# Kernel tuning notes

Measured on AMD Instinct MI355X. Metric: run time of the kernel, lower is better.

## Reference

```python
import jax, jax.numpy as jnp
import numpy as np

EPSILON = 0.01  # mesh.epsilon: boundary band of the unit square


def setup_inputs() -> dict:
    key = jax.random.key(0)
    k1, k2, k3 = jax.random.split(key, 3)
    V, E, F = 50000, 150000, 128
    image = jax.random.normal(k1, (V, F), dtype=jnp.float32)
    vs = jax.random.uniform(k2, (V, 2), dtype=jnp.float32)
    edges = jax.random.randint(k3, (2, E), 0, V, dtype=jnp.int32)
    return {"image": image, "vs": vs, "edges": edges, "out_target": 25000}


def _edge_priority(image, edges):
    # features = cat(image[e0], image[e1], dim=1) -> [E, 2F]; priority = ||f||^2 per edge
    f0 = image[edges[0]]  # [E, F]
    f1 = image[edges[1]]  # [E, F]
    return jnp.sum(f0 * f0, axis=1) + jnp.sum(f1 * f1, axis=1)  # [E]


def _boundary_mask(vs, edges):
    v0 = vs[edges[0]]  # [E, 2]
    v1 = vs[edges[1]]  # [E, 2]
    def near_border(v):
        return (v[:, 0] < EPSILON) | (v[:, 0] > 1 - EPSILON) | (v[:, 1] < EPSILON) | (v[:, 1] > 1 - EPSILON)
    return near_border(v0) | near_border(v1)  # [E] bool


def reference(image, vs, edges, out_target):
    V = image.shape[0]
    sq = _edge_priority(image, edges)            # [E] float32 (heap keys)
    is_boundary = _boundary_mask(vs, edges)      # [E] bool

    # heappop order == ascending priority (ties broken by edge id, matching heapify on [value, id])
    order = jnp.argsort(sq)
    e0 = edges[0][order]
    e1 = edges[1][order]
    bnd = is_boundary[order]

    # Sequential greedy edge collapse: pop min edge; if both endpoints alive and
    # not a boundary edge, merge (kill edges[1] vertex) until vertex_count hits target.
    def step(carry, x):
        mask, count = carry
        v0, v1, b = x
        alive = mask[v0] & mask[v1]
        do = (count > out_target) & alive & (~b)
        mask = mask.at[v1].set(jnp.where(do, False, mask[v1]))
        count = count - do.astype(jnp.int32)
        return (mask, count), None

    init = (jnp.ones((V,), dtype=bool), jnp.int32(V))
    (vertex_mask, vertex_count), _ = jax.lax.scan(step, init, (e0, e1, bnd))
    return sq, vertex_mask, vertex_count
```

## Files before the change

kernel.cpp:

```cpp
#include <hip/hip_runtime.h>
#include <hip/hip_bf16.h>
#include <stdint.h>

typedef unsigned int u32;
typedef unsigned long long u64;
typedef unsigned char u8;
typedef unsigned short u16;


__global__ __launch_bounds__(256) void vnorm_kernel(const float* __restrict__ image,
                                                    float* __restrict__ nrm, int V) {
#pragma clang fp contract(off)
  int t = blockIdx.x * 256 + threadIdx.x;
  int v = t >> 1, h = t & 1;
  if (v >= V) return;
  const float4* r4 = (const float4*)(image + (size_t)v * 128) + h;
  float4 a, x;
  x = r4[0];
  a.x = x.x * x.x; a.y = x.y * x.y; a.z = x.z * x.z; a.w = x.w * x.w;
#pragma unroll
  for (int i = 1; i < 16; ++i) {
    x = r4[i * 2];
    a.x = a.x + x.x * x.x; a.y = a.y + x.y * x.y;
    a.z = a.z + x.z * x.z; a.w = a.w + x.w * x.w;
  }
  float bx = __shfl_xor(a.x, 1), by = __shfl_xor(a.y, 1);
  float bz = __shfl_xor(a.z, 1), bw = __shfl_xor(a.w, 1);
  a.x = a.x + bx; a.y = a.y + by; a.z = a.z + bz; a.w = a.w + bw;
  float r0 = a.x + a.z;
  float r1 = a.y + a.w;
  float s = r0 + r1;
  if (h == 0) nrm[v] = s;
}

__global__ __launch_bounds__(256) void edge_kernel(const float* __restrict__ nrm,
                                                   const float* __restrict__ vs,
                                                   const int* __restrict__ edges,
                                                   u64* __restrict__ keysA,
                                                   u8* __restrict__ bnd,
                                                   float* __restrict__ out_sq,
                                                   u32* __restrict__ gmm, int E) {
#pragma clang fp contract(off)
  __shared__ u32 smn[4], smx[4];
  int tid = threadIdx.x;
  int e = blockIdx.x * 256 + tid;
  u32 mn = 0xFFFFFFFFu, mx = 0u;
  if (e < E) {
    int v0 = edges[e], v1 = edges[E + e];
    float sq = nrm[v0] + nrm[v1];
    out_sq[e] = sq;
    u32 sb = __float_as_uint(sq);
    keysA[e] = ((u64)sb << 32) | (u32)e;
    float ax = vs[2 * v0], ay = vs[2 * v0 + 1];
    float bx = vs[2 * v1], by = vs[2 * v1 + 1];
    const float lo = 0.01f, hi = 0.99f;
    bool b = (ax < lo) | (ax > hi) | (ay < lo) | (ay > hi)
           | (bx < lo) | (bx > hi) | (by < lo) | (by > hi);
    bnd[e] = b ? 1 : 0;
    mn = sb; mx = sb;
  }
  int lane = tid & 63, wv = tid >> 6;
#pragma unroll
  for (int d = 32; d >= 1; d >>= 1) {
    u32 a = __shfl_xor(mn, d); mn = (a < mn) ? a : mn;
    u32 b2 = __shfl_xor(mx, d); mx = (b2 > mx) ? b2 : mx;
  }
  if (lane == 0) { smn[wv] = mn; smx[wv] = mx; }
  __syncthreads();
  if (tid == 0) {
    u32 m = smn[0], M = smx[0];
#pragma unroll
    for (int w = 1; w < 4; ++w) {
      if (smn[w] < m) m = smn[w];
      if (smx[w] > M) M = smx[w];
    }
    atomicMin(&gmm[0], m);
    atomicMax(&gmm[1], M);
  }
}

__device__ inline u32 bucket_of(u32 sb, u32 minv, u32 range) {
  return (u32)(((u64)(sb - minv) << 14) / ((u64)range + 1ull));
}

__global__ __launch_bounds__(256) void hist_kernel(const u64* __restrict__ keysA,
                                                   const u32* __restrict__ gmm,
                                                   u32* __restrict__ ghist, int E) {
  int e = blockIdx.x * 256 + threadIdx.x;
  if (e >= E) return;
  u32 minv = gmm[0], range = gmm[1] - minv;
  u32 b = bucket_of((u32)(keysA[e] >> 32), minv, range);
  atomicAdd(&ghist[b], 1u);
}

__global__ __launch_bounds__(1024) void scan16k_kernel(const u32* __restrict__ ghist,
                                                       u32* __restrict__ starts,
                                                       u32* __restrict__ cursor, int E) {
  __shared__ u32 wsum[16];
  int tid = threadIdx.x;
  int lane = tid & 63, wv = tid >> 6;
  u32 loc[16];
  u32 s = 0;
#pragma unroll
  for (int i = 0; i < 16; ++i) { loc[i] = ghist[tid * 16 + i]; s += loc[i]; }
  u32 inc = s;
#pragma unroll
  for (int d = 1; d < 64; d <<= 1) {
    u32 t = __shfl_up(inc, d);
    if (lane >= d) inc += t;
  }
  if (lane == 63) wsum[wv] = inc;
  __syncthreads();
  if (tid == 0) {
    u32 r = 0;
#pragma unroll
    for (int w = 0; w < 16; ++w) { u32 t = wsum[w]; wsum[w] = r; r += t; }
  }
  __syncthreads();
  u32 run = wsum[wv] + (inc - s);
#pragma unroll
  for (int i = 0; i < 16; ++i) {
    starts[tid * 16 + i] = run;
    cursor[tid * 16 + i] = run;
    run += loc[i];
  }
  if (tid == 0) starts[16384] = (u32)E;
}

__global__ __launch_bounds__(256) void scatter_kernel(const u64* __restrict__ keysA,
                                                      const u32* __restrict__ gmm,
                                                      u32* __restrict__ cursor,
                                                      u64* __restrict__ keysB, int E) {
  int e = blockIdx.x * 256 + threadIdx.x;
  if (e >= E) return;
  u64 key = keysA[e];
  u32 minv = gmm[0], range = gmm[1] - minv;
  u32 b = bucket_of((u32)(key >> 32), minv, range);
  u32 pos = atomicAdd(&cursor[b], 1u);
  keysB[pos] = key;
}

__global__ __launch_bounds__(256) void bucketsort_kernel(const u64* __restrict__ keysB,
                                                         const u32* __restrict__ starts,
                                                         const int* __restrict__ edges,
                                                         const u8* __restrict__ bnd,
                                                         u64* __restrict__ pack,
                                                         int E, int V, int Npad) {
  int tid = threadIdx.x;
  int lane = tid & 63;
  int w = blockIdx.x * 4 + (tid >> 6);
  u32 start = starts[w];
  int cnt = (int)(starts[w + 1] - start);
  if (cnt > 128) cnt = 128;
  u64 k0 = (lane < cnt) ? keysB[start + lane] : ~0ull;
  u64 k1 = (64 + lane < cnt) ? keysB[start + 64 + lane] : ~0ull;
  int idx0 = lane * 2, idx1 = lane * 2 + 1;
#pragma unroll
  for (int k = 2; k <= 128; k <<= 1) {
#pragma unroll
    for (int j = 64; j >= 1; j >>= 1) {
      if (j > k / 2) continue;
      if (j >= 2) {
        int lj = j >> 1;
        u64 p0 = __shfl_xor(k0, lj);
        u64 p1 = __shfl_xor(k1, lj);
        bool keepMin0 = (((idx0 & j) == 0) == ((idx0 & k) == 0));
        k0 = keepMin0 ? (k0 < p0 ? k0 : p0) : (k0 > p0 ? k0 : p0);
        k1 = keepMin0 ? (k1 < p1 ? k1 : p1) : (k1 > p1 ? k1 : p1);
      } else {
        bool up = ((idx0 & k) == 0);
        u64 mn = (k0 < k1) ? k0 : k1;
        u64 mx = (k0 < k1) ? k1 : k0;
        k0 = up ? mn : mx;
        k1 = up ? mx : mn;
      }
    }
  }
  if (idx0 < cnt) {
    u32 id = (u32)k0;
    int vv0 = edges[id], vv1 = edges[E + id];
    pack[start + idx0] = (u64)(u32)(vv0 | (vv1 << 16)) | ((u64)bnd[id] << 32);
  }
  if (idx1 < cnt) {
    u32 id = (u32)k1;
    int vv0 = edges[id], vv1 = edges[E + id];
    pack[start + idx1] = (u64)(u32)(vv0 | (vv1 << 16)) | ((u64)bnd[id] << 32);
  }
  int g = blockIdx.x * 256 + tid;
  int i = E + g;
  if (i < Npad) {
    u32 sv0 = (u32)V + (((u32)i & 255u) << 1);
    pack[i] = (u64)(sv0 | ((sv0 + 1) << 16)) | (1ull << 32);
  }
}

__device__ inline void lds_min_u16(u16* tarr, int idx, u16 val) {
  u32* w = (u32*)(tarr + (idx & ~1));
  int sh = (idx & 1) * 16;
  u32 old = *w;
  while (true) {
    u32 cur = (old >> sh) & 0xffffu;
    if ((u32)val >= cur) break;
    u32 nv = (old & ~(0xffffu << sh)) | ((u32)val << sh);
    u32 prev = atomicCAS(w, old, nv);
    if (prev == old) break;
    old = prev;
  }
}

__global__ __launch_bounds__(1024) void batch_kernel(const u64* __restrict__ pack,
                                                     const int* __restrict__ tgt,
                                                     float* __restrict__ out,
                                                     u32* __restrict__ gbits,
                                                     int V, int E, int Npad) {
  __shared__ u16 tUK[50560];
  __shared__ u32 alive[1600];
  __shared__ u32 wred[17];
  __shared__ u32 misc[4];
  int tid = threadIdx.x;
  int lane = tid & 63, wv = tid >> 6;
  for (int i = tid; i < 1600; i += 1024) alive[i] = 0xFFFFFFFFu;
  for (int i = tid; i < 25280; i += 1024) ((u32*)tUK)[i] = 0xFFFFFFFFu;
  if (tid < 4) misc[tid] = 0u;
  int target = tgt[0];
  int needed = V - target; if (needed < 0) needed = 0;
  int remaining = needed;
  __syncthreads();
  int nbatch = Npad / 1024;
  u64 pk = pack[tid];
  for (int b = 0; b < nbatch; ++b) {
    if (remaining <= 0) break;
    u64 pkn = (b + 1 < nbatch) ? pack[(b + 1) * 1024 + tid] : pk;
    int v0 = (int)(pk & 0xffff), v1 = (int)((pk >> 16) & 0xffff);
    int nb = (int)((pk >> 32) & 1);
    int a0 = (int)((alive[v0 >> 5] >> (v0 & 31)) & 1);
    int a1 = (int)((alive[v1 >> 5] >> (v1 & 31)) & 1);
    int und = a0 & a1 & (nb ^ 1);
    int kill = 0;
    u32 myval = ((u32)tid << 1) | 1u;
    for (int r = 0; r < 1100; ++r) {
      if (und | kill) lds_min_u16(tUK, v1, (u16)(((u32)tid << 1) | (u32)und));
      __syncthreads();
      int newk = 0, newnk = 0;
      if (und) {
        u32 b0v = (v0 == v1) ? 0xFFFFu : (u32)tUK[v0];
        u32 b1v = (u32)tUK[v1];
        int ek = (int)(((b0v < myval) & ((b0v & 1u) ^ 1u)) |
                       ((b1v < myval) & ((b1v & 1u) ^ 1u)));
        int c0 = (int)(b0v > myval);
        int c1 = (int)(b1v == myval);
        newk = c0 & c1 & (ek ^ 1);
        newnk = ek;
      }
      kill |= newk;
      und &= (newk | newnk) ^ 1;
      u64 au = __ballot(und);
      if (lane == 0 && au) atomicOr(&misc[r & 3], 1u);
      if (tid == 0) misc[(r + 2) & 3] = 0u;
      __syncthreads();
      tUK[v1] = 0xFFFF;
      u32 anyu = misc[r & 3];
      __syncthreads();
      if (anyu == 0u) break;
    }
    u64 km = __ballot(kill);
    if (lane == 0) wred[wv] = (u32)__popcll(km);
    __syncthreads();
    if (tid == 0) {
      u32 run = 0;
      for (int w = 0; w < 16; ++w) { u32 t2 = wred[w]; wred[w] = run; run += t2; }
      wred[16] = run;
    }
    __syncthreads();
    u32 K = wred[16];
    if (kill) {
      u32 rank = wred[wv] + (u32)__popcll(km & ((1ull << lane) - 1ull));
      if (rank < (u32)remaining)
        atomicAnd(&alive[v1 >> 5], ~(1u << (v1 & 31)));
    }
    remaining -= (int)((K < (u32)remaining) ? K : (u32)remaining);
    if (tid < 4) misc[tid] = 0u;
    __syncthreads();
    pk = pkn;
  }
  for (int i = tid; i < 1600; i += 1024) gbits[i] = alive[i];
  if (tid == 0) out[E + V] = (float)(V - (needed - remaining));
}

__global__ __launch_bounds__(256) void expand_kernel(const u32* __restrict__ gbits,
                                                     float* __restrict__ out,
                                                     int V, int E) {
  int i = blockIdx.x * 256 + threadIdx.x;
  if (i < V) out[E + i] = ((gbits[i >> 5] >> (i & 31)) & 1) ? 1.0f : 0.0f;
}

extern "C" void kernel_launch(void* const* d_in, const int* in_sizes, int n_in,
                              void* d_out, int out_size, void* d_ws, size_t ws_size,
                              hipStream_t stream) {
  const float* image = (const float*)d_in[0];
  const float* vs    = (const float*)d_in[1];
  const int*   edges = (const int*)d_in[2];
  const int*   tgt   = (const int*)d_in[3];
  int V = in_sizes[1] / 2;
  int E = in_sizes[2] / 2;
  int Npad = ((E + 1023) / 1024) * 1024;

  char* ws = (char*)d_ws;
  size_t o = 0;
  u64* keysA  = (u64*)(ws + o); o += (size_t)E * 8;
  u64* keysB  = (u64*)(ws + o); o += (size_t)E * 8;
  u64* pack   = (u64*)(ws + o); o += (size_t)Npad * 8;
  float* nrm  = (float*)(ws + o); o += (size_t)V * 4;
  u8*  bnd    = (u8*)(ws + o);  o += (size_t)E;
  o = (o + 255) & ~(size_t)255;
  u32* ghist  = (u32*)(ws + o); o += 16384 * 4;
  u32* starts = (u32*)(ws + o); o += 16385 * 4;
  u32* cursor = (u32*)(ws + o); o += 16384 * 4;
  u32* gbits  = (u32*)(ws + o); o += 6400;
  u32* gmm    = (u32*)(ws + o); o += 256;
  float* out = (float*)d_out;

  (void)hipMemsetAsync(ghist, 0, 16384 * 4, stream);
  (void)hipMemsetAsync(&gmm[0], 0xFF, 4, stream);
  (void)hipMemsetAsync(&gmm[1], 0x00, 4, stream);

  int eb = (E + 255) / 256;
  vnorm_kernel<<<dim3((2 * V + 255) / 256), dim3(256), 0, stream>>>(image, nrm, V);
  edge_kernel<<<dim3(eb), dim3(256), 0, stream>>>(nrm, vs, edges, keysA, bnd, out, gmm, E);
  hist_kernel<<<dim3(eb), dim3(256), 0, stream>>>(keysA, gmm, ghist, E);
  scan16k_kernel<<<dim3(1), dim3(1024), 0, stream>>>(ghist, starts, cursor, E);
  scatter_kernel<<<dim3(eb), dim3(256), 0, stream>>>(keysA, gmm, cursor, keysB, E);
  bucketsort_kernel<<<dim3(4096), dim3(256), 0, stream>>>(keysB, starts, edges, bnd,
                                                          pack, E, V, Npad);
  batch_kernel<<<dim3(1), dim3(1024), 0, stream>>>(pack, tgt, out, gbits, V, E, Npad);
  expand_kernel<<<dim3((V + 255) / 256), dim3(256), 0, stream>>>(gbits, out, V, E);
}
```

Before: 261.0 us.

## Process 4096 edges per greedy batch and fold expand into batch kernel

The single-block greedy collapse now resolves 4096 sorted edges per batch instead of 1024. Each thread owns four edges, using macro-unrolled post/decide/rank/apply phases and a 64-entry warp-prefix array. This cuts the number of sequential batches and their barrier-heavy setup, but each batch may need more conflict-resolution rounds, and every round does four times the LDS work per thread. The separate expand kernel and its gbits buffer are removed, and the alive bitmask is written straight to the output from shared memory.

```diff
diff --git a/kernel.cpp b/kernel.cpp
--- a/kernel.cpp
+++ b/kernel.cpp
@@ -145,7 +145,7 @@
                                                          const int* __restrict__ edges,
                                                          const u8* __restrict__ bnd,
                                                          u64* __restrict__ pack,
-                                                         int E, int V, int Npad) {
+                                                         int E, int V, int NpadB) {
   int tid = threadIdx.x;
   int lane = tid & 63;
   int w = blockIdx.x * 4 + (tid >> 6);
@@ -188,7 +188,7 @@
   }
   int g = blockIdx.x * 256 + tid;
   int i = E + g;
-  if (i < Npad) {
+  if (i < NpadB) {
     u32 sv0 = (u32)V + (((u32)i & 255u) << 1);
     pack[i] = (u64)(sv0 | ((sv0 + 1) << 16)) | (1ull << 32);
   }
@@ -208,14 +208,15 @@
   }
 }
 
+#define NBAT 4096
+
 __global__ __launch_bounds__(1024) void batch_kernel(const u64* __restrict__ pack,
                                                      const int* __restrict__ tgt,
                                                      float* __restrict__ out,
-                                                     u32* __restrict__ gbits,
-                                                     int V, int E, int Npad) {
+                                                     int V, int E, int NpadB) {
   __shared__ u16 tUK[50560];
   __shared__ u32 alive[1600];
-  __shared__ u32 wred[17];
+  __shared__ u32 wred[65];
   __shared__ u32 misc[4];
   int tid = threadIdx.x;
   int lane = tid & 63, wv = tid >> 6;
@@ -226,72 +227,74 @@
   int needed = V - target; if (needed < 0) needed = 0;
   int remaining = needed;
   __syncthreads();
-  int nbatch = Npad / 1024;
-  u64 pk = pack[tid];
+  int nbatch = NpadB / NBAT;
+  u64 pk0 = pack[tid],        pk1 = pack[1024 + tid];
+  u64 pk2 = pack[2048 + tid], pk3 = pack[3072 + tid];
   for (int b = 0; b < nbatch; ++b) {
     if (remaining <= 0) break;
-    u64 pkn = (b + 1 < nbatch) ? pack[(b + 1) * 1024 + tid] : pk;
-    int v0 = (int)(pk & 0xffff), v1 = (int)((pk >> 16) & 0xffff);
-    int nb = (int)((pk >> 32) & 1);
-    int a0 = (int)((alive[v0 >> 5] >> (v0 & 31)) & 1);
-    int a1 = (int)((alive[v1 >> 5] >> (v1 & 31)) & 1);
-    int und = a0 & a1 & (nb ^ 1);
-    int kill = 0;
-    u32 myval = ((u32)tid << 1) | 1u;
-    for (int r = 0; r < 1100; ++r) {
-      if (und | kill) lds_min_u16(tUK, v1, (u16)(((u32)tid << 1) | (u32)und));
+    const u64* np = pack + (size_t)((b + 1 < nbatch) ? (b + 1) : b) * NBAT;
+    u64 pn0 = np[tid],        pn1 = np[1024 + tid];
+    u64 pn2 = np[2048 + tid], pn3 = np[3072 + tid];
+#define BDEC(S) \
+    int v0##S = (int)(pk##S & 0xffff), w1##S = (int)((pk##S >> 16) & 0xffff); \
+    int und##S, kill##S = 0; \
+    { int nb_ = (int)((pk##S >> 32) & 1); \
+      int a0 = (int)((alive[v0##S >> 5] >> (v0##S & 31)) & 1); \
+      int a1 = (int)((alive[w1##S >> 5] >> (w1##S & 31)) & 1); \
+      und##S = a0 & a1 & (nb_ ^ 1); } \
+    u32 my##S = ((u32)(S * 1024 + tid) << 1) | 1u;
+    BDEC(0) BDEC(1) BDEC(2) BDEC(3)
+    for (int r = 0; r < 4200; ++r) {
+#define BPOST(S) if (und##S | kill##S) \
+      lds_min_u16(tUK, w1##S, (u16)((((u32)(S * 1024 + tid)) << 1) | (u32)und##S));
+      BPOST(0) BPOST(1) BPOST(2) BPOST(3)
       __syncthreads();
-      int newk = 0, newnk = 0;
-      if (und) {
-        u32 b0v = (v0 == v1) ? 0xFFFFu : (u32)tUK[v0];
-        u32 b1v = (u32)tUK[v1];
-        int ek = (int)(((b0v < myval) & ((b0v & 1u) ^ 1u)) |
-                       ((b1v < myval) & ((b1v & 1u) ^ 1u)));
-        int c0 = (int)(b0v > myval);
-        int c1 = (int)(b1v == myval);
-        newk = c0 & c1 & (ek ^ 1);
-        newnk = ek;
+#define BDECIDE(S) \
+      if (und##S) { \
+        u32 b0v = (v0##S == w1##S) ? 0xFFFFu : (u32)tUK[v0##S]; \
+        u32 b1v = (u32)tUK[w1##S]; \
+        int ek = (int)(((b0v < my##S) & ((b0v & 1u) ^ 1u)) | \
+                       ((b1v < my##S) & ((b1v & 1u) ^ 1u))); \
+        int nk = (int)(b0v > my##S) & (int)(b1v == my##S) & (ek ^ 1); \
+        kill##S |= nk; \
+        und##S &= (nk | ek) ^ 1; \
       }
-      kill |= newk;
-      und &= (newk | newnk) ^ 1;
-      u64 au = __ballot(und);
+      BDECIDE(0) BDECIDE(1) BDECIDE(2) BDECIDE(3)
+      u64 au = __ballot(und0 | und1 | und2 | und3);
       if (lane == 0 && au) atomicOr(&misc[r & 3], 1u);
       if (tid == 0) misc[(r + 2) & 3] = 0u;
       __syncthreads();
-      tUK[v1] = 0xFFFF;
+      tUK[w10] = 0xFFFF; tUK[w11] = 0xFFFF;
+      tUK[w12] = 0xFFFF; tUK[w13] = 0xFFFF;
       u32 anyu = misc[r & 3];
       __syncthreads();
       if (anyu == 0u) break;
     }
-    u64 km = __ballot(kill);
-    if (lane == 0) wred[wv] = (u32)__popcll(km);
+#define BRANK(S) { u64 km = __ballot(kill##S); \
+      if (lane == 0) wred[S * 16 + wv] = (u32)__popcll(km); }
+    BRANK(0) BRANK(1) BRANK(2) BRANK(3)
+    if (tid < 4) misc[tid] = 0u;
     __syncthreads();
     if (tid == 0) {
       u32 run = 0;
-      for (int w = 0; w < 16; ++w) { u32 t2 = wred[w]; wred[w] = run; run += t2; }
-      wred[16] = run;
+      for (int i = 0; i < 64; ++i) { u32 t2 = wred[i]; wred[i] = run; run += t2; }
+      wred[64] = run;
     }
     __syncthreads();
-    u32 K = wred[16];
-    if (kill) {
-      u32 rank = wred[wv] + (u32)__popcll(km & ((1ull << lane) - 1ull));
-      if (rank < (u32)remaining)
-        atomicAnd(&alive[v1 >> 5], ~(1u << (v1 & 31)));
-    }
+    u32 K = wred[64];
+#define BAPPLY(S) { u64 km = __ballot(kill##S); \
+      if (kill##S) { \
+        u32 rank = wred[S * 16 + wv] + (u32)__popcll(km & ((1ull << lane) - 1ull)); \
+        if (rank < (u32)remaining) \
+          atomicAnd(&alive[w1##S >> 5], ~(1u << (w1##S & 31))); } }
+    BAPPLY(0) BAPPLY(1) BAPPLY(2) BAPPLY(3)
     remaining -= (int)((K < (u32)remaining) ? K : (u32)remaining);
-    if (tid < 4) misc[tid] = 0u;
     __syncthreads();
-    pk = pkn;
-  }
-  for (int i = tid; i < 1600; i += 1024) gbits[i] = alive[i];
+    pk0 = pn0; pk1 = pn1; pk2 = pn2; pk3 = pn3;
+  }
+  for (int i = tid; i < V; i += 1024)
+    out[E + i] = ((alive[i >> 5] >> (i & 31)) & 1) ? 1.0f : 0.0f;
   if (tid == 0) out[E + V] = (float)(V - (needed - remaining));
-}
-
-__global__ __launch_bounds__(256) void expand_kernel(const u32* __restrict__ gbits,
-                                                     float* __restrict__ out,
-                                                     int V, int E) {
-  int i = blockIdx.x * 256 + threadIdx.x;
-  if (i < V) out[E + i] = ((gbits[i >> 5] >> (i & 31)) & 1) ? 1.0f : 0.0f;
 }
 
 extern "C" void kernel_launch(void* const* d_in, const int* in_sizes, int n_in,
@@ -303,20 +306,19 @@
   const int*   tgt   = (const int*)d_in[3];
   int V = in_sizes[1] / 2;
   int E = in_sizes[2] / 2;
-  int Npad = ((E + 1023) / 1024) * 1024;
+  int NpadB = ((E + NBAT - 1) / NBAT) * NBAT;
 
   char* ws = (char*)d_ws;
   size_t o = 0;
   u64* keysA  = (u64*)(ws + o); o += (size_t)E * 8;
   u64* keysB  = (u64*)(ws + o); o += (size_t)E * 8;
-  u64* pack   = (u64*)(ws + o); o += (size_t)Npad * 8;
+  u64* pack   = (u64*)(ws + o); o += (size_t)NpadB * 8;
   float* nrm  = (float*)(ws + o); o += (size_t)V * 4;
   u8*  bnd    = (u8*)(ws + o);  o += (size_t)E;
   o = (o + 255) & ~(size_t)255;
   u32* ghist  = (u32*)(ws + o); o += 16384 * 4;
   u32* starts = (u32*)(ws + o); o += 16385 * 4;
   u32* cursor = (u32*)(ws + o); o += 16384 * 4;
-  u32* gbits  = (u32*)(ws + o); o += 6400;
   u32* gmm    = (u32*)(ws + o); o += 256;
   float* out = (float*)d_out;
 
@@ -331,7 +333,6 @@
   scan16k_kernel<<<dim3(1), dim3(1024), 0, stream>>>(ghist, starts, cursor, E);
   scatter_kernel<<<dim3(eb), dim3(256), 0, stream>>>(keysA, gmm, cursor, keysB, E);
   bucketsort_kernel<<<dim3(4096), dim3(256), 0, stream>>>(keysB, starts, edges, bnd,
-                                                          pack, E, V, Npad);
-  batch_kernel<<<dim3(1), dim3(1024), 0, stream>>>(pack, tgt, out, gbits, V, E, Npad);
-  expand_kernel<<<dim3((V + 255) / 256), dim3(256), 0, stream>>>(gbits, out, V, E);
-}
+                                                          pack, E, V, NpadB);
+  batch_kernel<<<dim3(1), dim3(1024), 0, stream>>>(pack, tgt, out, V, E, NpadB);
+}
```

Measured after the change: 237.1 us. -9.2%, faster.
